# Optimization experiments

Measured on AMD Instinct MI355X. Metric: run time of the kernel, lower is better.

Reference implementation:

```python
import jax, jax.numpy as jnp
import numpy as np

N = 40000       # nodes
E = 640000      # edges (before self-loops)
D_IN = 128      # input_dim
D = 128         # hidden_dim
HEADS = 8
C = D // HEADS  # per-head channels = 16
L = 3           # num_layers
G = 64          # number of graphs for mean pool
SLOPE = 0.2     # GATConv leaky_relu negative slope
EPS_LN = 1e-5


def setup_inputs() -> dict:
    key = jax.random.key(0)
    ks = jax.random.split(key, 12)
    x = jax.random.normal(ks[0], (N, D_IN), dtype=jnp.float32)
    edge_index = jax.random.randint(ks[1], (2, E), 0, N, dtype=jnp.int32)
    batch = jnp.sort(jax.random.randint(ks[2], (N,), 0, G, dtype=jnp.int32))
    s = 0.05
    return {
        "x": x,
        "edge_index": edge_index,
        "batch": batch,
        "W_in": jax.random.normal(ks[3], (D_IN, D), dtype=jnp.float32) * s,
        "b_in": jnp.zeros((D,), dtype=jnp.float32),
        "W_l": jax.random.normal(ks[4], (L, D, D), dtype=jnp.float32) * s,
        "att_src": jax.random.normal(ks[5], (L, HEADS, C), dtype=jnp.float32) * s,
        "att_dst": jax.random.normal(ks[6], (L, HEADS, C), dtype=jnp.float32) * s,
        "bias_l": jnp.zeros((L, D), dtype=jnp.float32),
        "gamma": jnp.ones((L, D), dtype=jnp.float32),
        "beta": jnp.zeros((L, D), dtype=jnp.float32),
    }


def _gat_layer(x, src, dst, W, a_s, a_d, b):
    n = x.shape[0]
    h = (x @ W).reshape(n, HEADS, C)            # [N,H,C]
    al_src = jnp.sum(h * a_s, axis=-1)          # [N,H]
    al_dst = jnp.sum(h * a_d, axis=-1)          # [N,H]
    logits = jax.nn.leaky_relu(al_src[src] + al_dst[dst], SLOPE)  # [Et,H]
    # segment softmax over incoming edges of each dst node
    m = jax.ops.segment_max(logits, dst, num_segments=n)
    m = jnp.where(jnp.isfinite(m), m, 0.0)
    e = jnp.exp(logits - m[dst])
    denom = jax.ops.segment_sum(e, dst, num_segments=n)
    alpha = e / (denom[dst] + 1e-16)            # [Et,H]
    msg = h[src] * alpha[:, :, None]            # [Et,H,C]
    out = jax.ops.segment_sum(msg, dst, num_segments=n)  # [N,H,C]
    return out.reshape(n, HEADS * C) + b


def _layer_norm(x, g, b):
    mu = jnp.mean(x, axis=-1, keepdims=True)
    var = jnp.var(x, axis=-1, keepdims=True)
    return (x - mu) * jax.lax.rsqrt(var + EPS_LN) * g + b


def reference(x, edge_index, batch, W_in, b_in, W_l, att_src, att_dst, bias_l, gamma, beta):
    n = x.shape[0]
    x = x @ W_in + b_in
    # add self loops (PyG GATConv default)
    loops = jnp.arange(n, dtype=edge_index.dtype)
    src = jnp.concatenate([edge_index[0], loops])
    dst = jnp.concatenate([edge_index[1], loops])
    for l in range(L):
        x = x + _gat_layer(x, src, dst, W_l[l], att_src[l], att_dst[l], bias_l[l])
        x = _layer_norm(x, gamma[l], beta[l])
        x = jax.nn.relu(x)
    # global mean pool over graph segments
    cnt = jax.ops.segment_sum(jnp.ones((n,), x.dtype), batch, num_segments=G)
    s = jax.ops.segment_sum(x, batch, num_segments=G)
    return s / jnp.maximum(cnt, 1.0)[:, None]
```

## Files before the change

kernel.cpp:

```cpp
#include <hip/hip_runtime.h>
#include <hip/hip_bf16.h>
#include <math.h>

#define NN 40000
#define DD 128
#define HH 8
#define EE 640000
#define ET (EE + NN)
#define GG 64
#define SLOPE 0.2f
#define CAP 64
#define NBKT 157
#define CAPB 6144
#define EPT 16

typedef unsigned int uint;
typedef unsigned short ushort;
typedef _Float16 f16x8 __attribute__((ext_vector_type(8)));
typedef __attribute__((ext_vector_type(4))) float f32x4;

__device__ inline ushort f2h(float f) {
    union { ushort s; _Float16 h; } c;
    c.h = (_Float16)f;
    return c.s;
}
__device__ inline float h_lo(uint u) {
    union { ushort s; _Float16 h; } c;
    c.s = (ushort)(u & 0xffffu);
    return (float)c.h;
}
__device__ inline float h_hi(uint u) {
    union { ushort s; _Float16 h; } c;
    c.s = (ushort)(u >> 16);
    return (float)c.h;
}

__global__ void zero_ws(int* __restrict__ gcnt, float* __restrict__ pool,
                        float* __restrict__ cnt) {
    int i = blockIdx.x * 256 + threadIdx.x;
    if (i < NBKT) gcnt[i] = 0;
    if (i < GG * DD) pool[i] = 0.f;
    if (i < GG) cnt[i] = 0.f;
}

__global__ void prep_wt(const float* __restrict__ Win, const float* __restrict__ Wl,
                        ushort* __restrict__ wt) {
    int i = blockIdx.x * 256 + threadIdx.x;
    if (i >= 4 * 128 * 128) return;
    int w = i >> 14, rem = i & 16383, n = rem >> 7, k = rem & 127;
    const float* src = (w == 0) ? Win : (Wl + (size_t)(w - 1) * 16384);
    wt[i] = f2h(src[k * 128 + n]);
}

__global__ __launch_bounds__(256) void bin_edges(const int* __restrict__ ei,
                                                 int* __restrict__ gcnt,
                                                 uint* __restrict__ bucket) {
    __shared__ int hist[NBKT];
    __shared__ int base[NBKT];
    int tid = threadIdx.x;
    int e0 = blockIdx.x * (256 * EPT);
    for (int j = tid; j < NBKT; j += 256) hist[j] = 0;
    __syncthreads();

    int la[EPT];
    #pragma unroll
    for (int i = 0; i < EPT; ++i) {
        int e = e0 + tid + i * 256;
        la[i] = -1;
        if (e < ET) {
            int d = (e < EE) ? ei[EE + e] : (e - EE);
            la[i] = atomicAdd(&hist[d >> 8], 1);
        }
    }
    __syncthreads();
    for (int j = tid; j < NBKT; j += 256) base[j] = atomicAdd(&gcnt[j], hist[j]);
    __syncthreads();

    #pragma unroll
    for (int i = 0; i < EPT; ++i) {
        int e = e0 + tid + i * 256;
        if (e < ET) {
            int s, d;
            if (e < EE) { s = ei[e]; d = ei[EE + e]; } else { s = d = e - EE; }
            int b = d >> 8;
            int pos = base[b] + la[i];
            if (pos < CAPB) bucket[b * CAPB + pos] = (uint)s | ((uint)(d & 255) << 16);
        }
    }
}

__global__ __launch_bounds__(256) void build_rows(const uint* __restrict__ bucket,
                                                  const int* __restrict__ gcnt,
                                                  ushort* __restrict__ colp,
                                                  int* __restrict__ deg) {
    __shared__ ushort cols[256 * 64];
    __shared__ int ldeg[256];
    int tid = threadIdx.x;
    int b = blockIdx.x;
    ldeg[tid] = 0;
    __syncthreads();
    int cnt = min(gcnt[b], CAPB);
    for (int i = tid; i < cnt; i += 256) {
        uint e = bucket[b * CAPB + i];
        int dl = e >> 16;
        int p = atomicAdd(&ldeg[dl], 1);
        if (p < CAP) cols[(dl << 6) + p] = (ushort)(e & 0xffffu);
    }
    __syncthreads();
    const uint4* src = (const uint4*)cols;
    for (int i = tid; i < 2048; i += 256) {
        int row = i >> 3;
        int n = (b << 8) + row;
        if (n < NN) ((uint4*)colp)[(size_t)n * 8 + (i & 7)] = src[i];
    }
    int n = (b << 8) + tid;
    if (n < NN) deg[n] = min(ldeg[tid], CAP);
}

__global__ __launch_bounds__(256) void gemm_mfma(const ushort* __restrict__ A16,
                                                 const float* __restrict__ Afp,
                                                 const ushort* __restrict__ WT,
                                                 const float* __restrict__ bias,
                                                 const float* __restrict__ atts,
                                                 const float* __restrict__ attd,
                                                 float* __restrict__ xout,
                                                 ushort* __restrict__ x16out,
                                                 float* __restrict__ al_s,
                                                 float* __restrict__ al_d,
                                                 ushort* __restrict__ h16out) {
    __shared__ ushort lds[128 * 136];
    int t = threadIdx.x;
    int wv = t >> 6, l = t & 63;
    int row0 = blockIdx.x * 64;

    {
        const uint4* src = (const uint4*)WT;
        for (int i = t; i < 2048; i += 256) {
            int r = i >> 4, c = i & 15;
            *(uint4*)((uint*)(lds + r * 136) + c * 4) = src[i];
        }
    }
    __syncthreads();

    int q = l >> 4, r16 = l & 15;
    f16x8 a0, a1, a2, a3;
    if (Afp) {
        const float* ar = Afp + (size_t)(row0 + wv * 16 + r16) * 128 + q * 8;
        {
            float4 fa = *(const float4*)(ar);
            float4 fb = *(const float4*)(ar + 4);
            a0 = (f16x8){(_Float16)fa.x, (_Float16)fa.y, (_Float16)fa.z, (_Float16)fa.w,
                         (_Float16)fb.x, (_Float16)fb.y, (_Float16)fb.z, (_Float16)fb.w};
        }
        {
            float4 fa = *(const float4*)(ar + 32);
            float4 fb = *(const float4*)(ar + 36);
            a1 = (f16x8){(_Float16)fa.x, (_Float16)fa.y, (_Float16)fa.z, (_Float16)fa.w,
                         (_Float16)fb.x, (_Float16)fb.y, (_Float16)fb.z, (_Float16)fb.w};
        }
        {
            float4 fa = *(const float4*)(ar + 64);
            float4 fb = *(const float4*)(ar + 68);
            a2 = (f16x8){(_Float16)fa.x, (_Float16)fa.y, (_Float16)fa.z, (_Float16)fa.w,
                         (_Float16)fb.x, (_Float16)fb.y, (_Float16)fb.z, (_Float16)fb.w};
        }
        {
            float4 fa = *(const float4*)(ar + 96);
            float4 fb = *(const float4*)(ar + 100);
            a3 = (f16x8){(_Float16)fa.x, (_Float16)fa.y, (_Float16)fa.z, (_Float16)fa.w,
                         (_Float16)fb.x, (_Float16)fb.y, (_Float16)fb.z, (_Float16)fb.w};
        }
    } else {
        const ushort* arow = A16 + (size_t)(row0 + wv * 16 + r16) * 128 + q * 8;
        a0 = *(const f16x8*)(arow);
        a1 = *(const f16x8*)(arow + 32);
        a2 = *(const f16x8*)(arow + 64);
        a3 = *(const f16x8*)(arow + 96);
    }
    f32x4 acc[8];
    #pragma unroll
    for (int c = 0; c < 8; ++c) acc[c] = (f32x4){0.f, 0.f, 0.f, 0.f};
    #pragma unroll
    for (int c = 0; c < 8; ++c) {
        const ushort* bp = lds + (c * 16 + r16) * 136 + q * 8;
        f16x8 b0 = *(const f16x8*)(bp);
        f16x8 b1 = *(const f16x8*)(bp + 32);
        f16x8 b2 = *(const f16x8*)(bp + 64);
        f16x8 b3 = *(const f16x8*)(bp + 96);
        acc[c] = __builtin_amdgcn_mfma_f32_16x16x32_f16(a0, b0, acc[c], 0, 0, 0);
        acc[c] = __builtin_amdgcn_mfma_f32_16x16x32_f16(a1, b1, acc[c], 0, 0, 0);
        acc[c] = __builtin_amdgcn_mfma_f32_16x16x32_f16(a2, b2, acc[c], 0, 0, 0);
        acc[c] = __builtin_amdgcn_mfma_f32_16x16x32_f16(a3, b3, acc[c], 0, 0, 0);
    }
    __syncthreads();

    float* tile = (float*)lds + wv * (16 * 132);
    #pragma unroll
    for (int c = 0; c < 8; ++c)
        #pragma unroll
        for (int i = 0; i < 4; ++i)
            tile[(q * 4 + i) * 132 + c * 16 + r16] = acc[c][i];
    __asm__ volatile("s_waitcnt lgkmcnt(0)" ::: "memory");

    #pragma unroll
    for (int uu = 0; uu < 2; ++uu) {
        int u = l + uu * 64;
        int row = u & 15, head = u >> 4;
        int n = row0 + wv * 16 + row;
        const float* rp = tile + row * 132 + head * 16;
        float4 h0 = *(const float4*)(rp);
        float4 h1 = *(const float4*)(rp + 4);
        float4 h2 = *(const float4*)(rp + 8);
        float4 h3 = *(const float4*)(rp + 12);
        if (h16out) {
            const float4* as4 = (const float4*)(atts + head * 16);
            const float4* ad4 = (const float4*)(attd + head * 16);
            float ss = 0.f, sd = 0.f;
            float4 a, b;
            a = as4[0]; b = ad4[0];
            ss += h0.x*a.x + h0.y*a.y + h0.z*a.z + h0.w*a.w;
            sd += h0.x*b.x + h0.y*b.y + h0.z*b.z + h0.w*b.w;
            a = as4[1]; b = ad4[1];
            ss += h1.x*a.x + h1.y*a.y + h1.z*a.z + h1.w*a.w;
            sd += h1.x*b.x + h1.y*b.y + h1.z*b.z + h1.w*b.w;
            a = as4[2]; b = ad4[2];
            ss += h2.x*a.x + h2.y*a.y + h2.z*a.z + h2.w*a.w;
            sd += h2.x*b.x + h2.y*b.y + h2.z*b.z + h2.w*b.w;
            a = as4[3]; b = ad4[3];
            ss += h3.x*a.x + h3.y*a.y + h3.z*a.z + h3.w*a.w;
            sd += h3.x*b.x + h3.y*b.y + h3.z*b.z + h3.w*b.w;
            al_s[(size_t)n * 8 + head] = ss;
            al_d[(size_t)n * 8 + head] = sd;
            uint4 p0, p1;
            p0.x = (uint)f2h(h0.x) | ((uint)f2h(h0.y) << 16);
            p0.y = (uint)f2h(h0.z) | ((uint)f2h(h0.w) << 16);
            p0.z = (uint)f2h(h1.x) | ((uint)f2h(h1.y) << 16);
            p0.w = (uint)f2h(h1.z) | ((uint)f2h(h1.w) << 16);
            p1.x = (uint)f2h(h2.x) | ((uint)f2h(h2.y) << 16);
            p1.y = (uint)f2h(h2.z) | ((uint)f2h(h2.w) << 16);
            p1.z = (uint)f2h(h3.x) | ((uint)f2h(h3.y) << 16);
            p1.w = (uint)f2h(h3.z) | ((uint)f2h(h3.w) << 16);
            uint4* dst = (uint4*)((uint*)h16out + (size_t)n * 64 + head * 8);
            dst[0] = p0; dst[1] = p1;
        } else {
            const float4* b4 = (const float4*)(bias + head * 16);
            float4 bb;
            bb = b4[0]; h0.x += bb.x; h0.y += bb.y; h0.z += bb.z; h0.w += bb.w;
            bb = b4[1]; h1.x += bb.x; h1.y += bb.y; h1.z += bb.z; h1.w += bb.w;
            bb = b4[2]; h2.x += bb.x; h2.y += bb.y; h2.z += bb.z; h2.w += bb.w;
            bb = b4[3]; h3.x += bb.x; h3.y += bb.y; h3.z += bb.z; h3.w += bb.w;
            float4* xo = (float4*)(xout + (size_t)n * 128 + head * 16);
            xo[0] = h0; xo[1] = h1; xo[2] = h2; xo[3] = h3;
            uint4 p0, p1;
            p0.x = (uint)f2h(h0.x) | ((uint)f2h(h0.y) << 16);
            p0.y = (uint)f2h(h0.z) | ((uint)f2h(h0.w) << 16);
            p0.z = (uint)f2h(h1.x) | ((uint)f2h(h1.y) << 16);
            p0.w = (uint)f2h(h1.z) | ((uint)f2h(h1.w) << 16);
            p1.x = (uint)f2h(h2.x) | ((uint)f2h(h2.y) << 16);
            p1.y = (uint)f2h(h2.z) | ((uint)f2h(h2.w) << 16);
            p1.z = (uint)f2h(h3.x) | ((uint)f2h(h3.y) << 16);
            p1.w = (uint)f2h(h3.z) | ((uint)f2h(h3.w) << 16);
            uint4* dst = (uint4*)((uint*)x16out + (size_t)n * 64 + head * 8);
            dst[0] = p0; dst[1] = p1;
        }
    }
}

__global__ __launch_bounds__(256) void gat_fused(const int* __restrict__ deg_a,
                                                 const ushort* __restrict__ colp,
                                                 const float* __restrict__ al_s,
                                                 const float* __restrict__ al_d,
                                                 const uint* __restrict__ h16,
                                                 const float* __restrict__ bias,
                                                 const float* __restrict__ gamma,
                                                 const float* __restrict__ beta,
                                                 float* __restrict__ x,
                                                 uint* __restrict__ x16u) {
    __shared__ float accv[4][128];
    int wv = threadIdx.x >> 6;
    int wave = blockIdx.x * 4 + wv;
    int lane = threadIdx.x & 63;
    if (wave >= NN) return;
    const int d = wave;
    const int deg = deg_a[d];

    const int gg = lane >> 4;
    const int cc = lane & 15;
    const int hd2 = cc >> 1;
    int col_r = 0;
    if (lane < deg) col_r = (int)colp[((size_t)d << 6) + lane];
    const float ald = al_d[(size_t)d * 8 + hd2];

    float ac[8] = {0.f, 0.f, 0.f, 0.f, 0.f, 0.f, 0.f, 0.f};
    float dsum = 0.f;
    for (int j = gg; j < deg; j += 4) {
        int s = __shfl(col_r, j);
        float tt = al_s[(size_t)s * 8 + hd2] + ald;
        tt = tt >= 0.f ? tt : SLOPE * tt;
        float e = __expf(tt);
        dsum += e;
        uint4 hv = *((const uint4*)(h16 + ((size_t)s << 6)) + cc);
        ac[0] += e * h_lo(hv.x); ac[1] += e * h_hi(hv.x);
        ac[2] += e * h_lo(hv.y); ac[3] += e * h_hi(hv.y);
        ac[4] += e * h_lo(hv.z); ac[5] += e * h_hi(hv.z);
        ac[6] += e * h_lo(hv.w); ac[7] += e * h_hi(hv.w);
    }
    #pragma unroll
    for (int i = 0; i < 8; ++i) {
        ac[i] += __shfl_xor(ac[i], 16);
        ac[i] += __shfl_xor(ac[i], 32);
    }
    dsum += __shfl_xor(dsum, 16);
    dsum += __shfl_xor(dsum, 32);
    float r = 1.f / (dsum + 1e-16f);
    if (gg == 0) {
        #pragma unroll
        for (int i2 = 0; i2 < 4; ++i2)
            *(float2*)&accv[wv][(cc << 3) + (i2 << 1)] =
                make_float2(ac[2 * i2] * r, ac[2 * i2 + 1] * r);
    }

    __asm__ volatile("s_waitcnt lgkmcnt(0)" ::: "memory");
    int colA = lane << 1;
    float2 av = *(const float2*)&accv[wv][colA];
    size_t base = (size_t)d * 128;
    float2 xv = *(const float2*)(x + base + colA);
    float2 bv = *(const float2*)(bias + colA);
    float v0 = xv.x + av.x + bv.x;
    float v1 = xv.y + av.y + bv.y;
    float sum = v0 + v1;
    #pragma unroll
    for (int off = 32; off; off >>= 1) sum += __shfl_xor(sum, off);
    float mu = sum * (1.f / 128.f);
    float d0 = v0 - mu, d1 = v1 - mu;
    float var = d0 * d0 + d1 * d1;
    #pragma unroll
    for (int off = 32; off; off >>= 1) var += __shfl_xor(var, off);
    float inv = rsqrtf(var * (1.f / 128.f) + 1e-5f);
    float2 gv = *(const float2*)(gamma + colA);
    float2 btv = *(const float2*)(beta + colA);
    float o0 = fmaxf((d0 * inv) * gv.x + btv.x, 0.f);
    float o1 = fmaxf((d1 * inv) * gv.y + btv.y, 0.f);
    *(float2*)(x + base + colA) = make_float2(o0, o1);
    if (x16u) x16u[(size_t)d * 64 + lane] = (uint)f2h(o0) | ((uint)f2h(o1) << 16);
}

__global__ __launch_bounds__(256) void pool_kernel(const float* __restrict__ x,
                                                   const int* __restrict__ batch,
                                                   float* __restrict__ s,
                                                   float* __restrict__ cnt) {
    __shared__ float acc[8][8][128];
    __shared__ float accc[8][8];
    const int NPB = 64;
    int t = threadIdx.x;
    int g = t >> 5;
    int lane = t & 31;
    int n0 = blockIdx.x * NPB;
    int nend = min(n0 + NPB, NN);
    int b0 = batch[n0];
    int span = batch[nend - 1] - b0 + 1;
    for (int i = t; i < 8 * 8 * 128; i += 256) ((float*)acc)[i] = 0.f;
    if (t < 64) ((float*)accc)[t] = 0.f;
    __syncthreads();
    if (span <= 8) {
        float4 r = make_float4(0.f, 0.f, 0.f, 0.f);
        float rc = 0.f;
        int cb = -1;
        for (int n = n0 + g; n < nend; n += 8) {
            int b = batch[n] - b0;
            if (b != cb) {
                if (cb >= 0) {
                    float4* p = (float4*)&acc[g][cb][lane * 4];
                    float4 cu = *p;
                    cu.x += r.x; cu.y += r.y; cu.z += r.z; cu.w += r.w;
                    *p = cu;
                    if (lane == 0) accc[g][cb] += rc;
                }
                r = make_float4(0.f, 0.f, 0.f, 0.f); rc = 0.f; cb = b;
            }
            float4 v = *(const float4*)(x + (size_t)n * 128 + lane * 4);
            r.x += v.x; r.y += v.y; r.z += v.z; r.w += v.w;
            rc += 1.f;
        }
        if (cb >= 0) {
            float4* p = (float4*)&acc[g][cb][lane * 4];
            float4 cu = *p;
            cu.x += r.x; cu.y += r.y; cu.z += r.z; cu.w += r.w;
            *p = cu;
            if (lane == 0) accc[g][cb] += rc;
        }
        __syncthreads();
        for (int i = t; i < span * 128; i += 256) {
            int b = i >> 7, c = i & 127;
            float v = 0.f;
            #pragma unroll
            for (int gq = 0; gq < 8; ++gq) v += acc[gq][b][c];
            atomicAdd(&s[(size_t)(b0 + b) * 128 + c], v);
        }
        if (t < span) {
            float v = 0.f;
            #pragma unroll
            for (int gq = 0; gq < 8; ++gq) v += accc[gq][t];
            atomicAdd(&cnt[b0 + t], v);
        }
    } else {
        int colc = t & 127, grp = t >> 7;
        for (int n = n0 + grp; n < nend; n += 2) {
            int b = batch[n];
            atomicAdd(&s[(size_t)b * 128 + colc], x[(size_t)n * 128 + colc]);
            if (colc == 0) atomicAdd(&cnt[b], 1.f);
        }
    }
}

__global__ void finalize_out(const float* __restrict__ s,
                             const float* __restrict__ cnt,
                             float* __restrict__ out) {
    int i = blockIdx.x * blockDim.x + threadIdx.x;
    if (i < GG * DD) out[i] = s[i] / fmaxf(cnt[i >> 7], 1.f);
}

extern "C" void kernel_launch(void* const* d_in, const int* in_sizes, int n_in,
                              void* d_out, int out_size, void* d_ws, size_t ws_size,
                              hipStream_t stream) {
    const float* x_in   = (const float*)d_in[0];
    const int*   ei     = (const int*)d_in[1];
    const int*   batch  = (const int*)d_in[2];
    const float* W_in   = (const float*)d_in[3];
    const float* b_in   = (const float*)d_in[4];
    const float* W_l    = (const float*)d_in[5];
    const float* att_s  = (const float*)d_in[6];
    const float* att_d  = (const float*)d_in[7];
    const float* bias_l = (const float*)d_in[8];
    const float* gamma  = (const float*)d_in[9];
    const float* beta   = (const float*)d_in[10];
    float* out = (float*)d_out;

    float* ws    = (float*)d_ws;
    float* xbuf  = ws;
    float* al_s  = xbuf + (size_t)NN * DD;
    float* al_d  = al_s + (size_t)NN * HH;
    float* pool  = al_d + (size_t)NN * HH;
    float* cnt   = pool + (size_t)GG * DD;
    int*   gcnt  = (int*)(cnt + GG);
    int*   deg   = gcnt + 160;
    uint*  bucket = (uint*)(deg + NN);
    ushort* colp = (ushort*)(bucket + (size_t)NBKT * CAPB);
    ushort* x16  = colp + (size_t)NN * CAP;
    ushort* h16  = x16 + (size_t)NN * 128;
    ushort* wt   = h16 + (size_t)NN * 128;

    zero_ws<<<(GG * DD + 255) / 256, 256, 0, stream>>>(gcnt, pool, cnt);
    bin_edges<<<(ET + 256 * EPT - 1) / (256 * EPT), 256, 0, stream>>>(ei, gcnt, bucket);
    build_rows<<<NBKT, 256, 0, stream>>>(bucket, gcnt, colp, deg);

    prep_wt<<<256, 256, 0, stream>>>(W_in, W_l, wt);

    gemm_mfma<<<625, 256, 0, stream>>>(nullptr, x_in, wt, b_in, nullptr, nullptr,
                                       xbuf, x16, nullptr, nullptr, nullptr);

    for (int l = 0; l < 3; ++l) {
        gemm_mfma<<<625, 256, 0, stream>>>(x16, nullptr, wt + (size_t)(1 + l) * 16384, nullptr,
                                           att_s + l * 128, att_d + l * 128,
                                           nullptr, nullptr, al_s, al_d, h16);
        gat_fused<<<NN / 4, 256, 0, stream>>>(deg, colp, al_s, al_d, (const uint*)h16,
                                              bias_l + l * 128, gamma + l * 128, beta + l * 128,
                                              xbuf, (l < 2) ? (uint*)x16 : nullptr);
    }

    pool_kernel<<<NN / 64, 256, 0, stream>>>(xbuf, batch, pool, cnt);
    finalize_out<<<(GG * DD + 255) / 256, 256, 0, stream>>>(pool, cnt, out);
}
```

Measured before the change: 207.3 us.

## Swap MFMA operands to write GEMM epilogue from registers and merge zero/prep kernels

The GEMM now feeds the weight fragment as the A operand and the activations as B, so each lane holds four consecutive output channels of one node. The epilogue writes fp16 h, the attention logits and the biased x straight from registers, using cross-lane shuffles for the per-head dot products. This removes the LDS transpose tile, a barrier and the LDS round trip. Separately, the workspace-zeroing kernel is merged into prep_wt, saving one launch. In exchange, global stores become narrower (8-byte uint2 per lane instead of 16-byte stores).

```diff
diff --git a/kernel.cpp b/kernel.cpp
--- a/kernel.cpp
+++ b/kernel.cpp
@@ -35,18 +35,13 @@
     return (float)c.h;
 }
 
-__global__ void zero_ws(int* __restrict__ gcnt, float* __restrict__ pool,
-                        float* __restrict__ cnt) {
+__global__ void prep_wt(const float* __restrict__ Win, const float* __restrict__ Wl,
+                        ushort* __restrict__ wt, int* __restrict__ gcnt,
+                        float* __restrict__ pool, float* __restrict__ cnt) {
     int i = blockIdx.x * 256 + threadIdx.x;
     if (i < NBKT) gcnt[i] = 0;
     if (i < GG * DD) pool[i] = 0.f;
     if (i < GG) cnt[i] = 0.f;
-}
-
-__global__ void prep_wt(const float* __restrict__ Win, const float* __restrict__ Wl,
-                        ushort* __restrict__ wt) {
-    int i = blockIdx.x * 256 + threadIdx.x;
-    if (i >= 4 * 128 * 128) return;
     int w = i >> 14, rem = i & 16383, n = rem >> 7, k = rem & 127;
     const float* src = (w == 0) ? Win : (Wl + (size_t)(w - 1) * 16384);
     wt[i] = f2h(src[k * 128 + n]);
@@ -142,126 +137,71 @@
     }
     __syncthreads();
 
-    int q = l >> 4, r16 = l & 15;
-    f16x8 a0, a1, a2, a3;
+    int q = l >> 4, j = l & 15;
+    int n = row0 + wv * 16 + j;
+
+    f16x8 xf[4];
     if (Afp) {
-        const float* ar = Afp + (size_t)(row0 + wv * 16 + r16) * 128 + q * 8;
-        {
-            float4 fa = *(const float4*)(ar);
-            float4 fb = *(const float4*)(ar + 4);
-            a0 = (f16x8){(_Float16)fa.x, (_Float16)fa.y, (_Float16)fa.z, (_Float16)fa.w,
-                         (_Float16)fb.x, (_Float16)fb.y, (_Float16)fb.z, (_Float16)fb.w};
-        }
-        {
-            float4 fa = *(const float4*)(ar + 32);
-            float4 fb = *(const float4*)(ar + 36);
-            a1 = (f16x8){(_Float16)fa.x, (_Float16)fa.y, (_Float16)fa.z, (_Float16)fa.w,
-                         (_Float16)fb.x, (_Float16)fb.y, (_Float16)fb.z, (_Float16)fb.w};
-        }
-        {
-            float4 fa = *(const float4*)(ar + 64);
-            float4 fb = *(const float4*)(ar + 68);
-            a2 = (f16x8){(_Float16)fa.x, (_Float16)fa.y, (_Float16)fa.z, (_Float16)fa.w,
-                         (_Float16)fb.x, (_Float16)fb.y, (_Float16)fb.z, (_Float16)fb.w};
-        }
-        {
-            float4 fa = *(const float4*)(ar + 96);
-            float4 fb = *(const float4*)(ar + 100);
-            a3 = (f16x8){(_Float16)fa.x, (_Float16)fa.y, (_Float16)fa.z, (_Float16)fa.w,
-                         (_Float16)fb.x, (_Float16)fb.y, (_Float16)fb.z, (_Float16)fb.w};
+        const float* ar = Afp + (size_t)n * 128 + q * 8;
+        #pragma unroll
+        for (int m = 0; m < 4; ++m) {
+            float4 fa = *(const float4*)(ar + m * 32);
+            float4 fb = *(const float4*)(ar + m * 32 + 4);
+            xf[m] = (f16x8){(_Float16)fa.x, (_Float16)fa.y, (_Float16)fa.z, (_Float16)fa.w,
+                            (_Float16)fb.x, (_Float16)fb.y, (_Float16)fb.z, (_Float16)fb.w};
         }
     } else {
-        const ushort* arow = A16 + (size_t)(row0 + wv * 16 + r16) * 128 + q * 8;
-        a0 = *(const f16x8*)(arow);
-        a1 = *(const f16x8*)(arow + 32);
-        a2 = *(const f16x8*)(arow + 64);
-        a3 = *(const f16x8*)(arow + 96);
-    }
+        const ushort* arow = A16 + (size_t)n * 128 + q * 8;
+        #pragma unroll
+        for (int m = 0; m < 4; ++m) xf[m] = *(const f16x8*)(arow + m * 32);
+    }
+
     f32x4 acc[8];
     #pragma unroll
     for (int c = 0; c < 8; ++c) acc[c] = (f32x4){0.f, 0.f, 0.f, 0.f};
     #pragma unroll
     for (int c = 0; c < 8; ++c) {
-        const ushort* bp = lds + (c * 16 + r16) * 136 + q * 8;
-        f16x8 b0 = *(const f16x8*)(bp);
-        f16x8 b1 = *(const f16x8*)(bp + 32);
-        f16x8 b2 = *(const f16x8*)(bp + 64);
-        f16x8 b3 = *(const f16x8*)(bp + 96);
-        acc[c] = __builtin_amdgcn_mfma_f32_16x16x32_f16(a0, b0, acc[c], 0, 0, 0);
-        acc[c] = __builtin_amdgcn_mfma_f32_16x16x32_f16(a1, b1, acc[c], 0, 0, 0);
-        acc[c] = __builtin_amdgcn_mfma_f32_16x16x32_f16(a2, b2, acc[c], 0, 0, 0);
-        acc[c] = __builtin_amdgcn_mfma_f32_16x16x32_f16(a3, b3, acc[c], 0, 0, 0);
-    }
-    __syncthreads();
-
-    float* tile = (float*)lds + wv * (16 * 132);
-    #pragma unroll
-    for (int c = 0; c < 8; ++c)
-        #pragma unroll
-        for (int i = 0; i < 4; ++i)
-            tile[(q * 4 + i) * 132 + c * 16 + r16] = acc[c][i];
-    __asm__ volatile("s_waitcnt lgkmcnt(0)" ::: "memory");
-
-    #pragma unroll
-    for (int uu = 0; uu < 2; ++uu) {
-        int u = l + uu * 64;
-        int row = u & 15, head = u >> 4;
-        int n = row0 + wv * 16 + row;
-        const float* rp = tile + row * 132 + head * 16;
-        float4 h0 = *(const float4*)(rp);
-        float4 h1 = *(const float4*)(rp + 4);
-        float4 h2 = *(const float4*)(rp + 8);
-        float4 h3 = *(const float4*)(rp + 12);
-        if (h16out) {
-            const float4* as4 = (const float4*)(atts + head * 16);
-            const float4* ad4 = (const float4*)(attd + head * 16);
-            float ss = 0.f, sd = 0.f;
-            float4 a, b;
-            a = as4[0]; b = ad4[0];
-            ss += h0.x*a.x + h0.y*a.y + h0.z*a.z + h0.w*a.w;
-            sd += h0.x*b.x + h0.y*b.y + h0.z*b.z + h0.w*b.w;
-            a = as4[1]; b = ad4[1];
-            ss += h1.x*a.x + h1.y*a.y + h1.z*a.z + h1.w*a.w;
-            sd += h1.x*b.x + h1.y*b.y + h1.z*b.z + h1.w*b.w;
-            a = as4[2]; b = ad4[2];
-            ss += h2.x*a.x + h2.y*a.y + h2.z*a.z + h2.w*a.w;
-            sd += h2.x*b.x + h2.y*b.y + h2.z*b.z + h2.w*b.w;
-            a = as4[3]; b = ad4[3];
-            ss += h3.x*a.x + h3.y*a.y + h3.z*a.z + h3.w*a.w;
-            sd += h3.x*b.x + h3.y*b.y + h3.z*b.z + h3.w*b.w;
-            al_s[(size_t)n * 8 + head] = ss;
-            al_d[(size_t)n * 8 + head] = sd;
-            uint4 p0, p1;
-            p0.x = (uint)f2h(h0.x) | ((uint)f2h(h0.y) << 16);
-            p0.y = (uint)f2h(h0.z) | ((uint)f2h(h0.w) << 16);
-            p0.z = (uint)f2h(h1.x) | ((uint)f2h(h1.y) << 16);
-            p0.w = (uint)f2h(h1.z) | ((uint)f2h(h1.w) << 16);
-            p1.x = (uint)f2h(h2.x) | ((uint)f2h(h2.y) << 16);
-            p1.y = (uint)f2h(h2.z) | ((uint)f2h(h2.w) << 16);
-            p1.z = (uint)f2h(h3.x) | ((uint)f2h(h3.y) << 16);
-            p1.w = (uint)f2h(h3.z) | ((uint)f2h(h3.w) << 16);
-            uint4* dst = (uint4*)((uint*)h16out + (size_t)n * 64 + head * 8);
-            dst[0] = p0; dst[1] = p1;
-        } else {
-            const float4* b4 = (const float4*)(bias + head * 16);
-            float4 bb;
-            bb = b4[0]; h0.x += bb.x; h0.y += bb.y; h0.z += bb.z; h0.w += bb.w;
-            bb = b4[1]; h1.x += bb.x; h1.y += bb.y; h1.z += bb.z; h1.w += bb.w;
-            bb = b4[2]; h2.x += bb.x; h2.y += bb.y; h2.z += bb.z; h2.w += bb.w;
-            bb = b4[3]; h3.x += bb.x; h3.y += bb.y; h3.z += bb.z; h3.w += bb.w;
-            float4* xo = (float4*)(xout + (size_t)n * 128 + head * 16);
-            xo[0] = h0; xo[1] = h1; xo[2] = h2; xo[3] = h3;
-            uint4 p0, p1;
-            p0.x = (uint)f2h(h0.x) | ((uint)f2h(h0.y) << 16);
-            p0.y = (uint)f2h(h0.z) | ((uint)f2h(h0.w) << 16);
-            p0.z = (uint)f2h(h1.x) | ((uint)f2h(h1.y) << 16);
-            p0.w = (uint)f2h(h1.z) | ((uint)f2h(h1.w) << 16);
-            p1.x = (uint)f2h(h2.x) | ((uint)f2h(h2.y) << 16);
-            p1.y = (uint)f2h(h2.z) | ((uint)f2h(h2.w) << 16);
-            p1.z = (uint)f2h(h3.x) | ((uint)f2h(h3.y) << 16);
-            p1.w = (uint)f2h(h3.z) | ((uint)f2h(h3.w) << 16);
-            uint4* dst = (uint4*)((uint*)x16out + (size_t)n * 64 + head * 8);
-            dst[0] = p0; dst[1] = p1;
+        const ushort* bp = lds + (c * 16 + j) * 136 + q * 8;
+        #pragma unroll
+        for (int m = 0; m < 4; ++m) {
+            f16x8 wf = *(const f16x8*)(bp + m * 32);
+            acc[c] = __builtin_amdgcn_mfma_f32_16x16x32_f16(wf, xf[m], acc[c], 0, 0, 0);
+        }
+    }
+
+    if (h16out) {
+        float ss[8], sd[8];
+        #pragma unroll
+        for (int c = 0; c < 8; ++c) {
+            float4 a = *(const float4*)(atts + c * 16 + q * 4);
+            float4 b = *(const float4*)(attd + c * 16 + q * 4);
+            float ps = acc[c][0]*a.x + acc[c][1]*a.y + acc[c][2]*a.z + acc[c][3]*a.w;
+            float pd = acc[c][0]*b.x + acc[c][1]*b.y + acc[c][2]*b.z + acc[c][3]*b.w;
+            ps += __shfl_xor(ps, 16); ps += __shfl_xor(ps, 32);
+            pd += __shfl_xor(pd, 16); pd += __shfl_xor(pd, 32);
+            ss[c] = ps; sd[c] = pd;
+            uint2 pk;
+            pk.x = (uint)f2h(acc[c][0]) | ((uint)f2h(acc[c][1]) << 16);
+            pk.y = (uint)f2h(acc[c][2]) | ((uint)f2h(acc[c][3]) << 16);
+            *(uint2*)(h16out + (size_t)n * 128 + c * 16 + q * 4) = pk;
+        }
+        if (q == 0) {
+            *(float4*)(al_s + (size_t)n * 8)     = make_float4(ss[0], ss[1], ss[2], ss[3]);
+            *(float4*)(al_s + (size_t)n * 8 + 4) = make_float4(ss[4], ss[5], ss[6], ss[7]);
+            *(float4*)(al_d + (size_t)n * 8)     = make_float4(sd[0], sd[1], sd[2], sd[3]);
+            *(float4*)(al_d + (size_t)n * 8 + 4) = make_float4(sd[4], sd[5], sd[6], sd[7]);
+        }
+    } else {
+        #pragma unroll
+        for (int c = 0; c < 8; ++c) {
+            float4 bb = *(const float4*)(bias + c * 16 + q * 4);
+            float4 o = make_float4(acc[c][0] + bb.x, acc[c][1] + bb.y,
+                                   acc[c][2] + bb.z, acc[c][3] + bb.w);
+            *(float4*)(xout + (size_t)n * 128 + c * 16 + q * 4) = o;
+            uint2 pk;
+            pk.x = (uint)f2h(o.x) | ((uint)f2h(o.y) << 16);
+            pk.y = (uint)f2h(o.z) | ((uint)f2h(o.w) << 16);
+            *(uint2*)(x16out + (size_t)n * 128 + c * 16 + q * 4) = pk;
         }
     }
 }
@@ -450,11 +390,9 @@
     ushort* h16  = x16 + (size_t)NN * 128;
     ushort* wt   = h16 + (size_t)NN * 128;
 
-    zero_ws<<<(GG * DD + 255) / 256, 256, 0, stream>>>(gcnt, pool, cnt);
+    prep_wt<<<256, 256, 0, stream>>>(W_in, W_l, wt, gcnt, pool, cnt);
     bin_edges<<<(ET + 256 * EPT - 1) / (256 * EPT), 256, 0, stream>>>(ei, gcnt, bucket);
     build_rows<<<NBKT, 256, 0, stream>>>(bucket, gcnt, colp, deg);
-
-    prep_wt<<<256, 256, 0, stream>>>(W_in, W_l, wt);
 
     gemm_mfma<<<625, 256, 0, stream>>>(nullptr, x_in, wt, b_in, nullptr, nullptr,
                                        xbuf, x16, nullptr, nullptr, nullptr);
```

After: 204.0 us (median of 2 runs). About the same (-1.6%).
